# Performance work log

Hardware: AMD Instinct MI355X
Metric: run time of the kernel (lower is better)

Reference implementation:

```python
import jax, jax.numpy as jnp
import numpy as np

N, M, FDIM, EDIM, H, HEADS = 8192, 8192, 128, 128, 64, 4
NEG = -1e9


def setup_inputs() -> dict:
    key = jax.random.key(0)
    ks = jax.random.split(key, 6)
    F0 = jax.random.normal(ks[0], (N, FDIM), dtype=jnp.float32)
    E0 = jax.random.normal(ks[1], (M, EDIM), dtype=jnp.float32)
    A = jax.random.randint(ks[2], (N, M), 0, 2, dtype=jnp.int32)
    Wf = jax.random.normal(ks[3], (HEADS, FDIM, H), dtype=jnp.float32) * 0.05
    We = jax.random.normal(ks[4], (HEADS, EDIM, H), dtype=jnp.float32) * 0.05
    a = jax.random.normal(ks[5], (HEADS, H), dtype=jnp.float32) * 0.05
    return {"F0": F0, "E0": E0, "A": A, "Wf": Wf, "We": We, "a": a}


def reference(F0, E0, A, Wf, We, a):
    # Per-head linear projections: h=head, n/m=nodes, d=hidden
    F1 = jnp.einsum('nf,hfd->hnd', F0, Wf)   # [H, N, D]
    E1 = jnp.einsum('me,hed->hmd', E0, We)   # [H, M, D]
    # Additive GAT scores: (h_src @ a) + (h_dst @ a), broadcast over the grid
    e_src = jnp.einsum('hnd,hd->hn', F1, a)  # [H, N]
    e_dst = jnp.einsum('hmd,hd->hm', E1, a)  # [H, M]
    e = jax.nn.leaky_relu(e_src[:, :, None] + e_dst[:, None, :], negative_slope=0.2)
    e = jnp.where(A[None, :, :] > 0, e, NEG)
    alpha = jax.nn.softmax(e, axis=-1)       # [H, N, M]
    h_prime = jnp.einsum('hnm,hmd->hnd', alpha, E1)  # [H, N, D]
    out = jnp.mean(h_prime, axis=0)          # mean over heads -> [N, D]
    return jax.nn.softmax(out, axis=-1)
```

## Files before the change

### kernel.cpp

```cpp
#include <hip/hip_runtime.h>
#include <hip/hip_fp16.h>

#define NN 8192
#define MM 8192
#define FD 128
#define EDm 128
#define HD 64
#define NH 4

typedef float f32x4 __attribute__((ext_vector_type(4)));
typedef _Float16 h16x8 __attribute__((ext_vector_type(8)));
typedef unsigned int u32;
typedef unsigned long long u64;

__global__ void k_prep(const int* __restrict__ A, u32* __restrict__ bitsG,
                       const float* __restrict__ F0, const float* __restrict__ Wf,
                       const float* __restrict__ aa, float* __restrict__ esrc,
                       const float* __restrict__ E0, const float* __restrict__ We,
                       uint4* __restrict__ Bp, _Float16* __restrict__ edh,
                       _Float16* __restrict__ ed2h) {
  __shared__ float vfL[NH * FD];
  const int bid = blockIdx.x;
  const int t = threadIdx.x;
  const int lane = t & 63;

  if (bid < 2048) {
    const int row = bid * 4 + (t >> 6);
    const int* ap = A + (size_t)row * MM + lane;
    u32* op = bitsG + (size_t)row * 256;
#pragma unroll 2
    for (int c = 0; c < 128; c += 8) {
      int v[8];
#pragma unroll
      for (int k = 0; k < 8; ++k)
        v[k] = __builtin_nontemporal_load(ap + (c + k) * 64);
      u64 b[8];
#pragma unroll
      for (int k = 0; k < 8; ++k) b[k] = __ballot(v[k] > 0);
      if (lane == 0) {
#pragma unroll
        for (int k = 0; k < 8; k += 2) {
          uint4 w = {(u32)b[k], (u32)(b[k] >> 32), (u32)b[k + 1], (u32)(b[k + 1] >> 32)};
          *(uint4*)(op + 2 * (c + k)) = w;
        }
      }
    }
  } else if (bid < 2176) {
    const int b2 = bid - 2048;
#pragma unroll
    for (int r = 0; r < 2; ++r) {
      int idx = t + r * 256;
      int h = idx >> 7, f = idx & 127;
      const float* w = Wf + (size_t)(h * FD + f) * HD;
      const float* av = aa + h * HD;
      float s = 0.f;
#pragma unroll
      for (int d = 0; d < HD; ++d) s += w[d] * av[d];
      vfL[idx] = s;
    }
    __syncthreads();
    int g = b2 * 256 + t;
    int n = g >> 2, h = g & 3;
    const float4* fr = (const float4*)(F0 + (size_t)n * FD);
    const float4* vr = (const float4*)(vfL + h * FD);
    float s = 0.f;
#pragma unroll
    for (int i = 0; i < FD / 4; ++i) {
      float4 x = fr[i], y = vr[i];
      s += x.x * y.x + x.y * y.y + x.z * y.z + x.w * y.w;
    }
    esrc[h * NN + n] = s;
  } else {
    const int wid = (bid - 2176) * 4 + (t >> 6);
    const int h = wid >> 10;
    const int mg = wid & 1023;
    const int m = mg * 8;
    const float* we = We + (size_t)h * EDm * HD + lane;
    const float* e0r = E0 + (size_t)m * EDm;
    float ac[8] = {};
#pragma unroll 4
    for (int e = 0; e < EDm; ++e) {
      float wv = we[e * HD];
#pragma unroll
      for (int j = 0; j < 8; ++j) ac[j] += e0r[j * EDm + e] * wv;
    }
    int mc = mg >> 2, quad = mg & 3, dt = lane >> 4, col = lane & 15;
    union { h16x8 v; uint4 u; } hv;
#pragma unroll
    for (int j = 0; j < 8; ++j) hv.v[j] = (_Float16)ac[j];
    Bp[(((size_t)h * 256 + mc) * 4 + dt) * 64 + quad * 16 + col] = hv.u;

    float av = aa[h * HD + lane];
    float d[8];
#pragma unroll
    for (int j = 0; j < 8; ++j) d[j] = ac[j] * av;
#pragma unroll
    for (int o = 32; o; o >>= 1)
#pragma unroll
      for (int j = 0; j < 8; ++j) d[j] += __shfl_xor(d[j], o);
    if (lane == 0) {
      const float L2E = 1.4426950408889634f;
      union { h16x8 v; uint4 u; } e1, e2;
#pragma unroll
      for (int j = 0; j < 8; ++j) {
        e1.v[j] = (_Float16)exp2f(d[j] * L2E);
        e2.v[j] = (_Float16)exp2f(0.2f * d[j] * L2E);
      }
      *(uint4*)(edh + (size_t)h * MM + m) = e1.u;
      *(uint4*)(ed2h + (size_t)h * MM + m) = e2.u;
    }
  }
}

__device__ __forceinline__ u32 hm2b(u32 w, int bit) {
  return (((w >> bit) & 1u) | (((w >> (bit + 1)) & 1u) << 16)) * 0xffffu;
}

__global__ __launch_bounds__(1024, 4) void k_main(
    const u32* __restrict__ bitsG, const uint4* __restrict__ Bp,
    const float* __restrict__ esrc, const _Float16* __restrict__ edh,
    const _Float16* __restrict__ ed2h, float* __restrict__ Npart,
    float* __restrict__ Dpart) {
  __shared__ __align__(16) u32 bits[128 * 68];

  const int t = threadIdx.x;
  const int lane = t & 63;
  const int wv = t >> 6;
  const int h = wv & 3;
  const int g = wv >> 2;
  const int col = lane & 15;
  const int quad = lane >> 4;
  const int qs = quad * 8;
  const int mq = blockIdx.x & 3;
  const int n0 = (blockIdx.x >> 2) * 128;
  const float L2E = 1.4426950408889634f;

#pragma unroll
  for (int i = 0; i < 2; ++i) {
    int idx = t + i * 1024;
    int row = idx >> 4, u4 = idx & 15;
    uint4 v = *(const uint4*)(bitsG + (size_t)(n0 + row) * 256 + mq * 64 + u4 * 4);
    *(uint4*)(bits + row * 68 + u4 * 4) = v;
  }

  const uint4* bp = Bp + (size_t)h * 65536 + (size_t)mq * 64 * 256 + lane;
  const _Float16* edp = edh + (size_t)h * MM + mq * 2048 + qs;
  const _Float16* e2p = ed2h + (size_t)h * MM + mq * 2048 + qs;

  uint4 bu0 = bp[0], bu1 = bp[64], bu2 = bp[128], bu3 = bp[192];
  h16x8 edv = *(const h16x8*)edp;
  h16x8 e2v = *(const h16x8*)e2p;

  float s0 = esrc[h * NN + n0 + g * 32 + col];
  float s1 = esrc[h * NN + n0 + g * 32 + 16 + col];
  _Float16 e80 = (_Float16)exp2f(0.8f * s0 * L2E);
  _Float16 e81 = (_Float16)exp2f(0.8f * s1 * L2E);
  h16x8 es80 = {e80, e80, e80, e80, e80, e80, e80, e80};
  h16x8 es81 = {e81, e81, e81, e81, e81, e81, e81, e81};
  const h16x8 ones = {(_Float16)1.f, (_Float16)1.f, (_Float16)1.f, (_Float16)1.f,
                      (_Float16)1.f, (_Float16)1.f, (_Float16)1.f, (_Float16)1.f};

  __syncthreads();

  const u32* rd0 = bits + (g * 32 + col) * 68;
  const u32* rd1 = bits + (g * 32 + 16 + col) * 68;
  u32 aw0 = rd0[0], aw1 = rd1[0];

  f32x4 acc[2][4] = {};
  f32x4 accd[2] = {};

  for (int it = 0; it < 64; ++it) {
    const int ip = (it < 63) ? it + 1 : 63;
    const u32 naw0 = rd0[ip];
    const u32 naw1 = rd1[ip];
    const uint4 nb0 = bp[ip * 256];
    const uint4 nb1 = bp[ip * 256 + 64];
    const uint4 nb2 = bp[ip * 256 + 128];
    const uint4 nb3 = bp[ip * 256 + 192];
    const h16x8 nedv = *(const h16x8*)(edp + ip * 32);
    const h16x8 ne2v = *(const h16x8*)(e2p + ip * 32);

    uint4 m0, m1;
    m0.x = hm2b(aw0, qs);     m0.y = hm2b(aw0, qs + 2);
    m0.z = hm2b(aw0, qs + 4); m0.w = hm2b(aw0, qs + 6);
    m1.x = hm2b(aw1, qs);     m1.y = hm2b(aw1, qs + 2);
    m1.z = hm2b(aw1, qs + 4); m1.w = hm2b(aw1, qs + 6);

    union { h16x8 v; uint4 u; } w0, w1, b0, b1, b2, b3;
    b0.u = bu0; b1.u = bu1; b2.u = bu2; b3.u = bu3;
    w0.v = __builtin_elementwise_max(edv * es80, e2v);
    w1.v = __builtin_elementwise_max(edv * es81, e2v);
    w0.u.x &= m0.x; w0.u.y &= m0.y; w0.u.z &= m0.z; w0.u.w &= m0.w;
    w1.u.x &= m1.x; w1.u.y &= m1.y; w1.u.z &= m1.z; w1.u.w &= m1.w;

    acc[0][0] = __builtin_amdgcn_mfma_f32_16x16x32_f16(w0.v, b0.v, acc[0][0], 0, 0, 0);
    acc[1][0] = __builtin_amdgcn_mfma_f32_16x16x32_f16(w1.v, b0.v, acc[1][0], 0, 0, 0);
    acc[0][1] = __builtin_amdgcn_mfma_f32_16x16x32_f16(w0.v, b1.v, acc[0][1], 0, 0, 0);
    acc[1][1] = __builtin_amdgcn_mfma_f32_16x16x32_f16(w1.v, b1.v, acc[1][1], 0, 0, 0);
    acc[0][2] = __builtin_amdgcn_mfma_f32_16x16x32_f16(w0.v, b2.v, acc[0][2], 0, 0, 0);
    acc[1][2] = __builtin_amdgcn_mfma_f32_16x16x32_f16(w1.v, b2.v, acc[1][2], 0, 0, 0);
    acc[0][3] = __builtin_amdgcn_mfma_f32_16x16x32_f16(w0.v, b3.v, acc[0][3], 0, 0, 0);
    acc[1][3] = __builtin_amdgcn_mfma_f32_16x16x32_f16(w1.v, b3.v, acc[1][3], 0, 0, 0);
    accd[0] = __builtin_amdgcn_mfma_f32_16x16x32_f16(w0.v, ones, accd[0], 0, 0, 0);
    accd[1] = __builtin_amdgcn_mfma_f32_16x16x32_f16(w1.v, ones, accd[1], 0, 0, 0);

    aw0 = naw0; aw1 = naw1; edv = nedv; e2v = ne2v;
    bu0 = nb0; bu1 = nb1; bu2 = nb2; bu3 = nb3;
  }

  float* np = Npart + (((size_t)(mq * 4 + h) * NN) + n0 + g * 32) * HD;
#pragma unroll
  for (int rt = 0; rt < 2; ++rt)
#pragma unroll
    for (int dt = 0; dt < 4; ++dt)
#pragma unroll
      for (int r2 = 0; r2 < 4; ++r2)
        np[(size_t)(rt * 16 + quad * 4 + r2) * HD + dt * 16 + col] = acc[rt][dt][r2];
  if (col == 0) {
    float* dp = Dpart + (size_t)(mq * 4 + h) * NN + n0 + g * 32;
#pragma unroll
    for (int rt = 0; rt < 2; ++rt)
#pragma unroll
      for (int r2 = 0; r2 < 4; ++r2)
        dp[rt * 16 + quad * 4 + r2] = accd[rt][r2];
  }
}

__global__ void k_comb(const float* __restrict__ Npart,
                       const float* __restrict__ Dpart,
                       float* __restrict__ out) {
  const int t = threadIdx.x;
  const int lane = t & 63;
  const int n = blockIdx.x * 4 + (t >> 6);
  const float L2E = 1.4426950408889634f;

  float v = 0.f;
#pragma unroll
  for (int h = 0; h < NH; ++h) {
    float num = 0.f, den = 0.f;
#pragma unroll
    for (int mq = 0; mq < 4; ++mq) {
      num += Npart[(((size_t)(mq * 4 + h) * NN) + n) * HD + lane];
      den += Dpart[(size_t)(mq * 4 + h) * NN + n];
    }
    v += num / den;
  }
  v *= 0.25f;

  float mx = v;
#pragma unroll
  for (int o = 32; o; o >>= 1) mx = fmaxf(mx, __shfl_xor(mx, o));
  float p = exp2f((v - mx) * L2E);
  float sm = p;
#pragma unroll
  for (int o = 32; o; o >>= 1) sm += __shfl_xor(sm, o);
  out[(size_t)n * HD + lane] = p / sm;
}

extern "C" void kernel_launch(void* const* d_in, const int* in_sizes, int n_in,
                              void* d_out, int out_size, void* d_ws, size_t ws_size,
                              hipStream_t stream) {
  const float* F0 = (const float*)d_in[0];
  const float* E0 = (const float*)d_in[1];
  const int* A = (const int*)d_in[2];
  const float* Wf = (const float*)d_in[3];
  const float* We = (const float*)d_in[4];
  const float* a = (const float*)d_in[5];
  float* out = (float*)d_out;

  char* w = (char*)d_ws;
  float* esrc = (float*)w;        w += (size_t)NH * NN * 4;
  _Float16* edh = (_Float16*)w;   w += (size_t)NH * MM * 2;
  _Float16* ed2h = (_Float16*)w;  w += (size_t)NH * MM * 2;
  uint4* Bp = (uint4*)w;          w += (size_t)NH * HD * MM * 2;
  u32* bitsG = (u32*)w;           w += (size_t)NN * 256 * 4;
  float* Npart = (float*)w;       w += (size_t)16 * NN * HD * 4;
  float* Dpart = (float*)w;       w += (size_t)16 * NN * 4;

  k_prep<<<3200, 256, 0, stream>>>(A, bitsG, F0, Wf, a, esrc, E0, We, Bp, edh, ed2h);
  k_main<<<256, 1024, 0, stream>>>(bitsG, Bp, esrc, edh, ed2h, Npart, Dpart);
  k_comb<<<NN / 4, 256, 0, stream>>>(Npart, Dpart, out);
}
```

Before: 453.1 us.

## Halve rows per block, drop register prefetch, compute denominator with VALU

Each k_main block now covers 64 rows instead of 128, so twice as many blocks launch (512) and each wave handles one 16-row tile. The manual next-iteration register prefetch is removed. The denominator MFMA against a ones vector is replaced by fp16 adds plus cross-lane shuffles, and launch bounds are raised to allow more waves per CU. The aim is better occupancy and CU fill (256 blocks likely underfilled the GPU). The cost is that each B fragment loaded from global memory now feeds half as many MFMAs, and fp16 partial sums in the denominator lose some precision.

```diff
diff --git a/kernel.cpp b/kernel.cpp
--- a/kernel.cpp
+++ b/kernel.cpp
@@ -116,12 +116,12 @@
   return (((w >> bit) & 1u) | (((w >> (bit + 1)) & 1u) << 16)) * 0xffffu;
 }
 
-__global__ __launch_bounds__(1024, 4) void k_main(
+__global__ __launch_bounds__(1024, 8) void k_main(
     const u32* __restrict__ bitsG, const uint4* __restrict__ Bp,
     const float* __restrict__ esrc, const _Float16* __restrict__ edh,
     const _Float16* __restrict__ ed2h, float* __restrict__ Npart,
     float* __restrict__ Dpart) {
-  __shared__ __align__(16) u32 bits[128 * 68];
+  __shared__ __align__(16) u32 bits[64 * 68];
 
   const int t = threadIdx.x;
   const int lane = t & 63;
@@ -132,98 +132,72 @@
   const int quad = lane >> 4;
   const int qs = quad * 8;
   const int mq = blockIdx.x & 3;
-  const int n0 = (blockIdx.x >> 2) * 128;
+  const int n0 = (blockIdx.x >> 2) * 64;
   const float L2E = 1.4426950408889634f;
 
-#pragma unroll
-  for (int i = 0; i < 2; ++i) {
-    int idx = t + i * 1024;
-    int row = idx >> 4, u4 = idx & 15;
+  {
+    int row = t >> 4, u4 = t & 15;
     uint4 v = *(const uint4*)(bitsG + (size_t)(n0 + row) * 256 + mq * 64 + u4 * 4);
     *(uint4*)(bits + row * 68 + u4 * 4) = v;
   }
 
-  const uint4* bp = Bp + (size_t)h * 65536 + (size_t)mq * 64 * 256 + lane;
+  const uint4* bp = Bp + (size_t)h * 65536 + (size_t)mq * 16384 + lane;
   const _Float16* edp = edh + (size_t)h * MM + mq * 2048 + qs;
   const _Float16* e2p = ed2h + (size_t)h * MM + mq * 2048 + qs;
 
-  uint4 bu0 = bp[0], bu1 = bp[64], bu2 = bp[128], bu3 = bp[192];
-  h16x8 edv = *(const h16x8*)edp;
-  h16x8 e2v = *(const h16x8*)e2p;
-
-  float s0 = esrc[h * NN + n0 + g * 32 + col];
-  float s1 = esrc[h * NN + n0 + g * 32 + 16 + col];
+  float s0 = esrc[h * NN + n0 + g * 16 + col];
   _Float16 e80 = (_Float16)exp2f(0.8f * s0 * L2E);
-  _Float16 e81 = (_Float16)exp2f(0.8f * s1 * L2E);
   h16x8 es80 = {e80, e80, e80, e80, e80, e80, e80, e80};
-  h16x8 es81 = {e81, e81, e81, e81, e81, e81, e81, e81};
-  const h16x8 ones = {(_Float16)1.f, (_Float16)1.f, (_Float16)1.f, (_Float16)1.f,
-                      (_Float16)1.f, (_Float16)1.f, (_Float16)1.f, (_Float16)1.f};
 
   __syncthreads();
 
-  const u32* rd0 = bits + (g * 32 + col) * 68;
-  const u32* rd1 = bits + (g * 32 + 16 + col) * 68;
-  u32 aw0 = rd0[0], aw1 = rd1[0];
-
-  f32x4 acc[2][4] = {};
-  f32x4 accd[2] = {};
+  const u32* rd0 = bits + (g * 16 + col) * 68;
+
+  f32x4 acc[4] = {};
+  float dacc = 0.f;
 
   for (int it = 0; it < 64; ++it) {
-    const int ip = (it < 63) ? it + 1 : 63;
-    const u32 naw0 = rd0[ip];
-    const u32 naw1 = rd1[ip];
-    const uint4 nb0 = bp[ip * 256];
-    const uint4 nb1 = bp[ip * 256 + 64];
-    const uint4 nb2 = bp[ip * 256 + 128];
-    const uint4 nb3 = bp[ip * 256 + 192];
-    const h16x8 nedv = *(const h16x8*)(edp + ip * 32);
-    const h16x8 ne2v = *(const h16x8*)(e2p + ip * 32);
-
-    uint4 m0, m1;
+    const u32 aw0 = rd0[it];
+    const uint4 b0u = bp[it * 256];
+    const uint4 b1u = bp[it * 256 + 64];
+    const uint4 b2u = bp[it * 256 + 128];
+    const uint4 b3u = bp[it * 256 + 192];
+    const h16x8 edv = *(const h16x8*)(edp + it * 32);
+    const h16x8 e2v = *(const h16x8*)(e2p + it * 32);
+
+    uint4 m0;
     m0.x = hm2b(aw0, qs);     m0.y = hm2b(aw0, qs + 2);
     m0.z = hm2b(aw0, qs + 4); m0.w = hm2b(aw0, qs + 6);
-    m1.x = hm2b(aw1, qs);     m1.y = hm2b(aw1, qs + 2);
-    m1.z = hm2b(aw1, qs + 4); m1.w = hm2b(aw1, qs + 6);
-
-    union { h16x8 v; uint4 u; } w0, w1, b0, b1, b2, b3;
-    b0.u = bu0; b1.u = bu1; b2.u = bu2; b3.u = bu3;
+
+    union { h16x8 v; uint4 u; } w0, b0, b1, b2, b3;
+    b0.u = b0u; b1.u = b1u; b2.u = b2u; b3.u = b3u;
     w0.v = __builtin_elementwise_max(edv * es80, e2v);
-    w1.v = __builtin_elementwise_max(edv * es81, e2v);
     w0.u.x &= m0.x; w0.u.y &= m0.y; w0.u.z &= m0.z; w0.u.w &= m0.w;
-    w1.u.x &= m1.x; w1.u.y &= m1.y; w1.u.z &= m1.z; w1.u.w &= m1.w;
-
-    acc[0][0] = __builtin_amdgcn_mfma_f32_16x16x32_f16(w0.v, b0.v, acc[0][0], 0, 0, 0);
-    acc[1][0] = __builtin_amdgcn_mfma_f32_16x16x32_f16(w1.v, b0.v, acc[1][0], 0, 0, 0);
-    acc[0][1] = __builtin_amdgcn_mfma_f32_16x16x32_f16(w0.v, b1.v, acc[0][1], 0, 0, 0);
-    acc[1][1] = __builtin_amdgcn_mfma_f32_16x16x32_f16(w1.v, b1.v, acc[1][1], 0, 0, 0);
-    acc[0][2] = __builtin_amdgcn_mfma_f32_16x16x32_f16(w0.v, b2.v, acc[0][2], 0, 0, 0);
-    acc[1][2] = __builtin_amdgcn_mfma_f32_16x16x32_f16(w1.v, b2.v, acc[1][2], 0, 0, 0);
-    acc[0][3] = __builtin_amdgcn_mfma_f32_16x16x32_f16(w0.v, b3.v, acc[0][3], 0, 0, 0);
-    acc[1][3] = __builtin_amdgcn_mfma_f32_16x16x32_f16(w1.v, b3.v, acc[1][3], 0, 0, 0);
-    accd[0] = __builtin_amdgcn_mfma_f32_16x16x32_f16(w0.v, ones, accd[0], 0, 0, 0);
-    accd[1] = __builtin_amdgcn_mfma_f32_16x16x32_f16(w1.v, ones, accd[1], 0, 0, 0);
-
-    aw0 = naw0; aw1 = naw1; edv = nedv; e2v = ne2v;
-    bu0 = nb0; bu1 = nb1; bu2 = nb2; bu3 = nb3;
-  }
-
-  float* np = Npart + (((size_t)(mq * 4 + h) * NN) + n0 + g * 32) * HD;
-#pragma unroll
-  for (int rt = 0; rt < 2; ++rt)
-#pragma unroll
-    for (int dt = 0; dt < 4; ++dt)
-#pragma unroll
-      for (int r2 = 0; r2 < 4; ++r2)
-        np[(size_t)(rt * 16 + quad * 4 + r2) * HD + dt * 16 + col] = acc[rt][dt][r2];
-  if (col == 0) {
-    float* dp = Dpart + (size_t)(mq * 4 + h) * NN + n0 + g * 32;
-#pragma unroll
-    for (int rt = 0; rt < 2; ++rt)
-#pragma unroll
-      for (int r2 = 0; r2 < 4; ++r2)
-        dp[rt * 16 + quad * 4 + r2] = accd[rt][r2];
-  }
+
+    acc[0] = __builtin_amdgcn_mfma_f32_16x16x32_f16(w0.v, b0.v, acc[0], 0, 0, 0);
+    acc[1] = __builtin_amdgcn_mfma_f32_16x16x32_f16(w0.v, b1.v, acc[1], 0, 0, 0);
+    acc[2] = __builtin_amdgcn_mfma_f32_16x16x32_f16(w0.v, b2.v, acc[2], 0, 0, 0);
+    acc[3] = __builtin_amdgcn_mfma_f32_16x16x32_f16(w0.v, b3.v, acc[3], 0, 0, 0);
+
+    _Float16 a0 = w0.v[0] + w0.v[4];
+    _Float16 a1 = w0.v[1] + w0.v[5];
+    _Float16 a2 = w0.v[2] + w0.v[6];
+    _Float16 a3 = w0.v[3] + w0.v[7];
+    _Float16 c0 = a0 + a2, c1 = a1 + a3;
+    dacc += (float)c0 + (float)c1;
+  }
+
+  float* np = Npart + (((size_t)(mq * 4 + h) * NN) + n0 + g * 16) * HD;
+#pragma unroll
+  for (int dt = 0; dt < 4; ++dt)
+#pragma unroll
+    for (int r2 = 0; r2 < 4; ++r2)
+      np[(size_t)(quad * 4 + r2) * HD + dt * 16 + col] = acc[dt][r2];
+
+  dacc += __shfl_xor(dacc, 16);
+  dacc += __shfl_xor(dacc, 32);
+  if (quad == 0)
+    Dpart[(size_t)(mq * 4 + h) * NN + n0 + g * 16 + col] = dacc;
 }
 
 __global__ void k_comb(const float* __restrict__ Npart,
@@ -278,6 +252,6 @@
   float* Dpart = (float*)w;       w += (size_t)16 * NN * 4;
 
   k_prep<<<3200, 256, 0, stream>>>(A, bitsG, F0, Wf, a, esrc, E0, We, Bp, edh, ed2h);
-  k_main<<<256, 1024, 0, stream>>>(bitsG, Bp, esrc, edh, ed2h, Npart, Dpart);
+  k_main<<<512, 1024, 0, stream>>>(bitsG, Bp, esrc, edh, ed2h, Npart, Dpart);
   k_comb<<<NN / 4, 256, 0, stream>>>(Npart, Dpart, out);
 }
```

After: 493.2 us. 8.9% more time.

## Give each wave 64 rows and compute row sums with VALU instead of MFMA

Applied to the files above, without the earlier changes.

Blocks shrink from 1024 to 512 threads, and each wave now handles 64 rows (four 16-row tiles) instead of 32. Each B-fragment load from global memory therefore feeds twice as many MFMAs, which halves B traffic per row. The denominator MFMA against a ones vector is replaced by fp16 adds plus a cross-lane shuffle reduction. This removes 2 of the 10 MFMAs per iteration but adds VALU work, fp16 partial-sum rounding, and more accumulator registers, which can lower occupancy.

```diff
diff --git a/kernel.cpp b/kernel.cpp
--- a/kernel.cpp
+++ b/kernel.cpp
@@ -116,7 +116,7 @@
   return (((w >> bit) & 1u) | (((w >> (bit + 1)) & 1u) << 16)) * 0xffffu;
 }
 
-__global__ __launch_bounds__(1024, 4) void k_main(
+__global__ __launch_bounds__(512, 2) void k_main(
     const u32* __restrict__ bitsG, const uint4* __restrict__ Bp,
     const float* __restrict__ esrc, const _Float16* __restrict__ edh,
     const _Float16* __restrict__ ed2h, float* __restrict__ Npart,
@@ -136,14 +136,14 @@
   const float L2E = 1.4426950408889634f;
 
 #pragma unroll
-  for (int i = 0; i < 2; ++i) {
-    int idx = t + i * 1024;
+  for (int i = 0; i < 4; ++i) {
+    int idx = t + i * 512;
     int row = idx >> 4, u4 = idx & 15;
     uint4 v = *(const uint4*)(bitsG + (size_t)(n0 + row) * 256 + mq * 64 + u4 * 4);
     *(uint4*)(bits + row * 68 + u4 * 4) = v;
   }
 
-  const uint4* bp = Bp + (size_t)h * 65536 + (size_t)mq * 64 * 256 + lane;
+  const uint4* bp = Bp + (size_t)h * 65536 + (size_t)mq * 16384 + lane;
   const _Float16* edp = edh + (size_t)h * MM + mq * 2048 + qs;
   const _Float16* e2p = ed2h + (size_t)h * MM + mq * 2048 + qs;
 
@@ -151,78 +151,82 @@
   h16x8 edv = *(const h16x8*)edp;
   h16x8 e2v = *(const h16x8*)e2p;
 
-  float s0 = esrc[h * NN + n0 + g * 32 + col];
-  float s1 = esrc[h * NN + n0 + g * 32 + 16 + col];
-  _Float16 e80 = (_Float16)exp2f(0.8f * s0 * L2E);
-  _Float16 e81 = (_Float16)exp2f(0.8f * s1 * L2E);
-  h16x8 es80 = {e80, e80, e80, e80, e80, e80, e80, e80};
-  h16x8 es81 = {e81, e81, e81, e81, e81, e81, e81, e81};
-  const h16x8 ones = {(_Float16)1.f, (_Float16)1.f, (_Float16)1.f, (_Float16)1.f,
-                      (_Float16)1.f, (_Float16)1.f, (_Float16)1.f, (_Float16)1.f};
+  h16x8 es8v[4];
+#pragma unroll
+  for (int r = 0; r < 4; ++r) {
+    float s = esrc[h * NN + n0 + g * 64 + r * 16 + col];
+    _Float16 e8 = (_Float16)exp2f(0.8f * s * L2E);
+    h16x8 sp = {e8, e8, e8, e8, e8, e8, e8, e8};
+    es8v[r] = sp;
+  }
 
   __syncthreads();
 
-  const u32* rd0 = bits + (g * 32 + col) * 68;
-  const u32* rd1 = bits + (g * 32 + 16 + col) * 68;
-  u32 aw0 = rd0[0], aw1 = rd1[0];
-
-  f32x4 acc[2][4] = {};
-  f32x4 accd[2] = {};
+  u32 aw[4];
+#pragma unroll
+  for (int r = 0; r < 4; ++r) aw[r] = bits[(g * 64 + r * 16 + col) * 68];
+
+  f32x4 acc[4][4] = {};
+  float dacc[4] = {};
 
   for (int it = 0; it < 64; ++it) {
     const int ip = (it < 63) ? it + 1 : 63;
-    const u32 naw0 = rd0[ip];
-    const u32 naw1 = rd1[ip];
     const uint4 nb0 = bp[ip * 256];
     const uint4 nb1 = bp[ip * 256 + 64];
     const uint4 nb2 = bp[ip * 256 + 128];
     const uint4 nb3 = bp[ip * 256 + 192];
     const h16x8 nedv = *(const h16x8*)(edp + ip * 32);
     const h16x8 ne2v = *(const h16x8*)(e2p + ip * 32);
-
-    uint4 m0, m1;
-    m0.x = hm2b(aw0, qs);     m0.y = hm2b(aw0, qs + 2);
-    m0.z = hm2b(aw0, qs + 4); m0.w = hm2b(aw0, qs + 6);
-    m1.x = hm2b(aw1, qs);     m1.y = hm2b(aw1, qs + 2);
-    m1.z = hm2b(aw1, qs + 4); m1.w = hm2b(aw1, qs + 6);
-
-    union { h16x8 v; uint4 u; } w0, w1, b0, b1, b2, b3;
+    u32 naw[4];
+#pragma unroll
+    for (int r = 0; r < 4; ++r) naw[r] = bits[(g * 64 + r * 16 + col) * 68 + ip];
+
+    union { h16x8 v; uint4 u; } b0, b1, b2, b3;
     b0.u = bu0; b1.u = bu1; b2.u = bu2; b3.u = bu3;
-    w0.v = __builtin_elementwise_max(edv * es80, e2v);
-    w1.v = __builtin_elementwise_max(edv * es81, e2v);
-    w0.u.x &= m0.x; w0.u.y &= m0.y; w0.u.z &= m0.z; w0.u.w &= m0.w;
-    w1.u.x &= m1.x; w1.u.y &= m1.y; w1.u.z &= m1.z; w1.u.w &= m1.w;
-
-    acc[0][0] = __builtin_amdgcn_mfma_f32_16x16x32_f16(w0.v, b0.v, acc[0][0], 0, 0, 0);
-    acc[1][0] = __builtin_amdgcn_mfma_f32_16x16x32_f16(w1.v, b0.v, acc[1][0], 0, 0, 0);
-    acc[0][1] = __builtin_amdgcn_mfma_f32_16x16x32_f16(w0.v, b1.v, acc[0][1], 0, 0, 0);
-    acc[1][1] = __builtin_amdgcn_mfma_f32_16x16x32_f16(w1.v, b1.v, acc[1][1], 0, 0, 0);
-    acc[0][2] = __builtin_amdgcn_mfma_f32_16x16x32_f16(w0.v, b2.v, acc[0][2], 0, 0, 0);
-    acc[1][2] = __builtin_amdgcn_mfma_f32_16x16x32_f16(w1.v, b2.v, acc[1][2], 0, 0, 0);
-    acc[0][3] = __builtin_amdgcn_mfma_f32_16x16x32_f16(w0.v, b3.v, acc[0][3], 0, 0, 0);
-    acc[1][3] = __builtin_amdgcn_mfma_f32_16x16x32_f16(w1.v, b3.v, acc[1][3], 0, 0, 0);
-    accd[0] = __builtin_amdgcn_mfma_f32_16x16x32_f16(w0.v, ones, accd[0], 0, 0, 0);
-    accd[1] = __builtin_amdgcn_mfma_f32_16x16x32_f16(w1.v, ones, accd[1], 0, 0, 0);
-
-    aw0 = naw0; aw1 = naw1; edv = nedv; e2v = ne2v;
+
+#pragma unroll
+    for (int r = 0; r < 4; ++r) {
+      uint4 m;
+      m.x = hm2b(aw[r], qs);     m.y = hm2b(aw[r], qs + 2);
+      m.z = hm2b(aw[r], qs + 4); m.w = hm2b(aw[r], qs + 6);
+
+      union { h16x8 v; uint4 u; } w;
+      w.v = __builtin_elementwise_max(edv * es8v[r], e2v);
+      w.u.x &= m.x; w.u.y &= m.y; w.u.z &= m.z; w.u.w &= m.w;
+
+      acc[r][0] = __builtin_amdgcn_mfma_f32_16x16x32_f16(w.v, b0.v, acc[r][0], 0, 0, 0);
+      acc[r][1] = __builtin_amdgcn_mfma_f32_16x16x32_f16(w.v, b1.v, acc[r][1], 0, 0, 0);
+      acc[r][2] = __builtin_amdgcn_mfma_f32_16x16x32_f16(w.v, b2.v, acc[r][2], 0, 0, 0);
+      acc[r][3] = __builtin_amdgcn_mfma_f32_16x16x32_f16(w.v, b3.v, acc[r][3], 0, 0, 0);
+
+      _Float16 a0 = w.v[0] + w.v[4];
+      _Float16 a1 = w.v[1] + w.v[5];
+      _Float16 a2 = w.v[2] + w.v[6];
+      _Float16 a3 = w.v[3] + w.v[7];
+      _Float16 c0 = a0 + a2, c1 = a1 + a3;
+      dacc[r] += (float)c0 + (float)c1;
+    }
+
+#pragma unroll
+    for (int r = 0; r < 4; ++r) aw[r] = naw[r];
+    edv = nedv; e2v = ne2v;
     bu0 = nb0; bu1 = nb1; bu2 = nb2; bu3 = nb3;
   }
 
-  float* np = Npart + (((size_t)(mq * 4 + h) * NN) + n0 + g * 32) * HD;
-#pragma unroll
-  for (int rt = 0; rt < 2; ++rt)
+#pragma unroll
+  for (int r = 0; r < 4; ++r) {
+    float* np = Npart + (((size_t)(mq * 4 + h) * NN) + n0 + g * 64 + r * 16) * HD;
 #pragma unroll
     for (int dt = 0; dt < 4; ++dt)
 #pragma unroll
       for (int r2 = 0; r2 < 4; ++r2)
-        np[(size_t)(rt * 16 + quad * 4 + r2) * HD + dt * 16 + col] = acc[rt][dt][r2];
-  if (col == 0) {
-    float* dp = Dpart + (size_t)(mq * 4 + h) * NN + n0 + g * 32;
-#pragma unroll
-    for (int rt = 0; rt < 2; ++rt)
-#pragma unroll
-      for (int r2 = 0; r2 < 4; ++r2)
-        dp[rt * 16 + quad * 4 + r2] = accd[rt][r2];
+        np[(size_t)(quad * 4 + r2) * HD + dt * 16 + col] = acc[r][dt][r2];
+
+    float d = dacc[r];
+    d += __shfl_xor(d, 16);
+    d += __shfl_xor(d, 32);
+    if (quad == 0)
+      Dpart[(size_t)(mq * 4 + h) * NN + n0 + g * 64 + r * 16 + col] = d;
   }
 }
 
@@ -278,6 +282,6 @@
   float* Dpart = (float*)w;       w += (size_t)16 * NN * 4;
 
   k_prep<<<3200, 256, 0, stream>>>(A, bitsG, F0, Wf, a, esrc, E0, We, Bp, edh, ed2h);
-  k_main<<<256, 1024, 0, stream>>>(bitsG, Bp, esrc, edh, ed2h, Npart, Dpart);
+  k_main<<<256, 512, 0, stream>>>(bitsG, Bp, esrc, edh, ed2h, Npart, Dpart);
   k_comb<<<NN / 4, 256, 0, stream>>>(Npart, Dpart, out);
 }
```

New measurement: 462.9 us. +2.2%, slower.
